# Kernel tuning notes

Hardware: AMD Instinct MI355X
Metric: run time of the kernel (lower is better)

## Reference

```python
import jax, jax.numpy as jnp
import numpy as np

NPG = 39      # nodes per graph, from (1+8+64+9)*(39+1)=3280 = lin1 in_features
NEG_SLOPE = 0.2


def gat_conv(x, src, dst, W, a_src, a_dst, b, n):
    """PyG GATConv, heads=1, self-loops already appended to (src, dst).
    x:[N,Fin] W:[Fin,Fout] a_src/a_dst:[Fout] b:[Fout] -> [N,Fout]"""
    h = x @ W                                        # [N,Fout]
    e = jax.nn.leaky_relu(h[src] @ a_src + h[dst] @ a_dst, NEG_SLOPE)  # [E]
    m = jax.lax.stop_gradient(jax.ops.segment_max(e, dst, num_segments=n))
    w = jnp.exp(e - m[dst])
    denom = jax.ops.segment_sum(w, dst, num_segments=n)
    alpha = w / (denom[dst] + 1e-16)                 # segment softmax per target node
    out = jax.ops.segment_sum(alpha[:, None] * h[src], dst, num_segments=n)
    return out + b


def setup_inputs() -> dict:
    key = jax.random.key(0)
    ks = jax.random.split(key, 20)
    B, DEG = 4096, 8
    N = B * NPG
    E = N * DEG
    x = jax.random.normal(ks[0], (N, 1), dtype=jnp.float32)
    # block-diagonal edges: each node emits DEG edges to random nodes in SAME graph
    src = jnp.repeat(jnp.arange(N, dtype=jnp.int64), DEG)
    offs = (src // NPG) * NPG
    dst = offs + jax.random.randint(ks[1], (E,), 0, NPG, dtype=jnp.int64)
    edge_index = jnp.stack([src, dst])
    batch_vec = jnp.repeat(jnp.arange(B, dtype=jnp.int64), NPG)

    def glorot(k, shape):
        fan = shape[0] + (shape[1] if len(shape) > 1 else 1)
        s = jnp.sqrt(6.0 / fan)
        return jax.random.uniform(k, shape, jnp.float32, -s, s)

    p = {
        'W1': glorot(ks[2], (1, 8)),   'a1s': glorot(ks[3], (8,)),  'a1d': glorot(ks[4], (8,)),  'b1': jnp.zeros((8,), jnp.float32),
        'W2': glorot(ks[5], (8, 64)),  'a2s': glorot(ks[6], (64,)), 'a2d': glorot(ks[7], (64,)), 'b2': jnp.zeros((64,), jnp.float32),
        'W3': glorot(ks[8], (64, 9)),  'a3s': glorot(ks[9], (9,)),  'a3d': glorot(ks[10], (9,)), 'b3': jnp.zeros((9,), jnp.float32),
        'lW1': glorot(ks[11], (3280, 5000)), 'lb1': jnp.zeros((5000,), jnp.float32),
        'lW2': glorot(ks[12], (5000, 1024)), 'lb2': jnp.zeros((1024,), jnp.float32),
        'lW3': glorot(ks[13], (1024, 9)),    'lb3': jnp.zeros((9,), jnp.float32),
    }
    return {'x': x, 'edge_index': edge_index, 'batch_vec': batch_vec, **p}


def reference(x, edge_index, batch_vec,
              W1, a1s, a1d, b1, W2, a2s, a2d, b2, W3, a3s, a3d, b3,
              lW1, lb1, lW2, lb2, lW3, lb3):
    N = x.shape[0]
    B = N // NPG
    loops = jnp.arange(N, dtype=edge_index.dtype)
    src = jnp.concatenate([edge_index[0], loops])   # GATConv add_self_loops=True
    dst = jnp.concatenate([edge_index[1], loops])

    res = x.reshape(B, -1)                                    # [B,39]
    out0 = jax.ops.segment_max(x, batch_vec, num_segments=B)  # [B,1]

    h1 = jax.nn.relu(gat_conv(x, src, dst, W1, a1s, a1d, b1, N))   # dropout = eval no-op
    res1 = h1.reshape(B, -1)                                   # [B,312]
    out1 = jax.ops.segment_max(h1, batch_vec, num_segments=B)

    h2 = jax.nn.relu(gat_conv(h1, src, dst, W2, a2s, a2d, b2, N))
    res2 = h2.reshape(B, -1)                                   # [B,2496]
    out2 = jax.ops.segment_max(h2, batch_vec, num_segments=B)

    h3 = jax.nn.relu(gat_conv(h2, src, dst, W3, a3s, a3d, b3, N))
    res3 = h3.reshape(B, -1)                                   # [B,351]
    out3 = jax.ops.segment_max(h3, batch_vec, num_segments=B)

    f = jnp.concatenate([res, res1, res2, res3, out0, out1, out2, out3], axis=1)  # [B,3280]
    f = jax.nn.relu(f @ lW1 + lb1)
    f = jax.nn.relu(f @ lW2 + lb2)
    return f @ lW3 + lb3                                       # [B,9]
```

## Files before the change

kernel.cpp:

```cpp
#include <hip/hip_runtime.h>
#include <hip/hip_bf16.h>
#include <hip/hip_fp16.h>
#include <stdint.h>


typedef float f32x4 __attribute__((ext_vector_type(4)));
typedef short bf16x8 __attribute__((ext_vector_type(8)));
typedef _Float16 f16x8 __attribute__((ext_vector_type(8)));

__device__ __forceinline__ unsigned fenc(float f) {
  int s = __float_as_int(f);
  return s < 0 ? ~(unsigned)s : ((unsigned)s | 0x80000000u);
}
__device__ __forceinline__ float fdec(unsigned u) {
  return (u & 0x80000000u) ? __int_as_float((int)(u & 0x7fffffffu))
                           : __int_as_float(~(int)u);
}


__global__ __launch_bounds__(128) void gnn_block(
    const float* __restrict__ x,
    const int* __restrict__ esrc, const int* __restrict__ edst,
    const float* __restrict__ W1, const float* __restrict__ a1s, const float* __restrict__ a1d, const float* __restrict__ b1,
    const float* __restrict__ W2, const float* __restrict__ a2s, const float* __restrict__ a2d, const float* __restrict__ b2,
    const float* __restrict__ W3, const float* __restrict__ a3s, const float* __restrict__ a3d, const float* __restrict__ b3,
    __hip_bfloat16* __restrict__ fA)
{
  __shared__ __align__(16) float A[1720];
  __shared__ __align__(16) __half Hh2[2816];
  __shared__ __align__(16) __half h1h[320];
  __shared__ __align__(16) float HfT[400];
  __shared__ __align__(16) float sW3T[616];
  __shared__ __align__(16) float xbuf[40];
  __shared__ __align__(16) float a2buf[128];
  __shared__ float sarr[40], darr[40], den[40];
  __shared__ unsigned umax[40];
  __shared__ unsigned umx[132];
  __shared__ float a3sb[12], a3db[12], b3b[12];

  const int tid = threadIdx.x, g = blockIdx.x, w = tid >> 6, f = tid & 63;

  const int rt = g >> 7, mi = (g >> 4) & 7, lrow = g & 15;
  const size_t gbase = (size_t)rt * 52 * 8192 + (size_t)(mi * 2) * 512 + (size_t)lrow * 8;
#define COLADDR(c) (gbase + (size_t)((c) >> 6) * 8192 + (size_t)(((c) >> 5) & 1) * 512 \
                    + (size_t)(((c) >> 3) & 3) * 128 + ((c) & 7))

  for (int i = tid; i < 576; i += 128) { int k = i / 9, f3 = i - 9 * k; sW3T[f3 * 68 + k] = W3[i]; }
  a2buf[tid] = (tid < 64) ? a2s[tid] : a2d[tid - 64];
  if (tid < 9) { a3sb[tid] = a3s[tid]; a3db[tid] = a3d[tid]; b3b[tid] = b3[tid]; }
  for (int i = tid; i < 132; i += 128) umx[i] = 0u;
  for (int i = tid; i < 430; i += 128) *(f32x4*)&A[i * 4] = (f32x4){0.f, 0.f, 0.f, 0.f};
  for (int i = tid; i < 400; i += 128) HfT[i] = 0.f;
  if (tid < 40) { den[tid] = 0.f; umax[tid] = 0u; xbuf[tid] = 0.f; }

  float xv = 0.f;
  if (tid < 39) { xv = x[g * 39 + tid]; xbuf[tid] = xv; fA[COLADDR(tid)] = __float2bfloat16(xv); }

  int els[3], eld[3];
  const int eb = g * 312, nb0 = g * 39;
#pragma unroll
  for (int it = 0; it < 3; ++it) {
    int e = it * 128 + tid, ls = -1, ld = 0;
    if (e < 351) {
      if (e < 312) { ls = esrc[eb + e] - nb0; ld = edst[eb + e] - nb0; }
      else         { ls = e - 312; ld = ls; }
    }
    els[it] = ls; eld[it] = ld;
  }
  float c_s = 0.f, c_d = 0.f;
  const float w1r = W1[tid & 7], b1r = b1[tid & 7];
#pragma unroll
  for (int ff = 0; ff < 8; ++ff) { float wv = W1[ff]; c_s += wv * a1s[ff]; c_d += wv * a1d[ff]; }
  __syncthreads();

  if (tid < 39) atomicMax(&umx[0], fenc(xv));
  float ee[3];
#pragma unroll
  for (int it = 0; it < 3; ++it) {
    if (els[it] >= 0) {
      float e = xbuf[els[it]] * c_s + xbuf[eld[it]] * c_d;
      e = (e > 0.f) ? e : 0.2f * e;
      ee[it] = e;
      atomicMax(&umax[eld[it]], fenc(e));
    }
  }
  __syncthreads();
#pragma unroll
  for (int it = 0; it < 3; ++it) {
    if (els[it] >= 0) {
      float wv = __expf(ee[it] - fdec(umax[eld[it]]));
      atomicAdd(&den[eld[it]], wv);
      atomicAdd(&A[eld[it] * 44 + els[it]], wv);
    }
  }
  __syncthreads();
  if (tid < 39) {
    const float* Ar = &A[tid * 44];
    float q = 0.f;
#pragma unroll
    for (int c = 0; c < 10; ++c) {
      f32x4 a4 = *(const f32x4*)&Ar[c * 4];
      f32x4 x4 = *(const f32x4*)&xbuf[c * 4];
      q += a4.x * x4.x + a4.y * x4.y + a4.z * x4.z + a4.w * x4.w;
    }
    sarr[tid] = q * (1.f / (den[tid] + 1e-16f));
  }
  __syncthreads();
#pragma unroll
  for (int it = 0; it < 3; ++it) {
    int slot = it * 128 + tid;
    if (slot < 312) {
      int i = slot >> 3, fi = slot & 7;
      float v = fmaxf(sarr[i] * w1r + b1r, 0.f);
      h1h[slot] = __float2half(v);
      fA[COLADDR(39 + slot)] = __float2bfloat16(v);
      atomicMax(&umx[1 + fi], fenc(v));
    }
  }
  __syncthreads();

  float ht2r[40];
  {
    float w2k[8];
#pragma unroll
    for (int k = 0; k < 8; ++k) w2k[k] = W2[k * 64 + f];
#pragma unroll
    for (int i = 0; i < 39; ++i) {
      f16x8 hr = *(const f16x8*)&h1h[i * 8];
      float hv = 0.f;
#pragma unroll
      for (int k = 0; k < 8; ++k) hv += (float)hr[k] * w2k[k];
      ht2r[i] = hv;
    }
    ht2r[39] = 0.f;
#pragma unroll
    for (int i = 0; i < 39; ++i) {
      if ((i < 20) ? (w == 0) : (w == 1))
        Hh2[i * 72 + f] = __float2half(ht2r[i]);
    }
    for (int i = tid; i < 430; i += 128) *(f32x4*)&A[i * 4] = (f32x4){0.f, 0.f, 0.f, 0.f};
    if (tid < 39) { den[tid] = 0.f; umax[tid] = 0u; }
  }
  __syncthreads();
  {
    int node = f;
    if (node < 39) {
      const float* ab = a2buf + (tid & 64);
      const __half* hr = &Hh2[node * 72];
      float s = 0.f;
#pragma unroll
      for (int c = 0; c < 8; ++c) {
        f16x8 hv = *(const f16x8*)&hr[c * 8];
        f32x4 a0 = *(const f32x4*)&ab[c * 8];
        f32x4 a1 = *(const f32x4*)&ab[c * 8 + 4];
        s += (float)hv[0] * a0.x + (float)hv[1] * a0.y + (float)hv[2] * a0.z + (float)hv[3] * a0.w
           + (float)hv[4] * a1.x + (float)hv[5] * a1.y + (float)hv[6] * a1.z + (float)hv[7] * a1.w;
      }
      if (tid < 64) sarr[node] = s; else darr[node] = s;
    }
  }
  __syncthreads();
#pragma unroll
  for (int it = 0; it < 3; ++it) {
    if (els[it] >= 0) {
      float e = sarr[els[it]] + darr[eld[it]];
      e = (e > 0.f) ? e : 0.2f * e;
      ee[it] = e;
      atomicMax(&umax[eld[it]], fenc(e));
    }
  }
  __syncthreads();
#pragma unroll
  for (int it = 0; it < 3; ++it) {
    if (els[it] >= 0) {
      float wv = __expf(ee[it] - fdec(umax[eld[it]]));
      atomicAdd(&den[eld[it]], wv);
      atomicAdd(&A[eld[it] * 44 + els[it]], wv);
    }
  }
  __syncthreads();
  {
    const float b2r = b2[f];
    for (int it = 0; it < 20; ++it) {
      int i = it * 2 + w;
      if (i < 39) {
        float inv = 1.f / (den[i] + 1e-16f);
        const float* Ar = &A[i * 44];
        float acc = 0.f;
#pragma unroll
        for (int c = 0; c < 10; ++c) {
          f32x4 a4 = *(const f32x4*)&Ar[c * 4];
          acc += a4.x * ht2r[c * 4] + a4.y * ht2r[c * 4 + 1]
               + a4.z * ht2r[c * 4 + 2] + a4.w * ht2r[c * 4 + 3];
        }
        float v = fmaxf(acc * inv + b2r, 0.f);
        Hh2[i * 72 + f] = __float2half(v);
        fA[COLADDR(351 + i * 64 + f)] = __float2bfloat16(v);
        atomicMax(&umx[9 + f], fenc(v));
      }
    }
  }
  __syncthreads();

  {
#pragma unroll
    for (int it = 0; it < 3; ++it) {
      int slot = it * 128 + tid;
      if (slot < 351) {
        int i = slot / 9, f3 = slot - 9 * i;
        const __half* hr = &Hh2[i * 72];
        const float* wr = &sW3T[f3 * 68];
        float acc = 0.f;
#pragma unroll
        for (int c = 0; c < 8; ++c) {
          f16x8 hv = *(const f16x8*)&hr[c * 8];
          f32x4 w0 = *(const f32x4*)&wr[c * 8];
          f32x4 w1 = *(const f32x4*)&wr[c * 8 + 4];
          acc += (float)hv[0] * w0.x + (float)hv[1] * w0.y + (float)hv[2] * w0.z + (float)hv[3] * w0.w
               + (float)hv[4] * w1.x + (float)hv[5] * w1.y + (float)hv[6] * w1.z + (float)hv[7] * w1.w;
        }
        HfT[f3 * 44 + i] = acc;
      }
    }
    for (int i = tid; i < 430; i += 128) *(f32x4*)&A[i * 4] = (f32x4){0.f, 0.f, 0.f, 0.f};
    if (tid < 39) { den[tid] = 0.f; umax[tid] = 0u; }
  }
  __syncthreads();
  {
    int node = f;
    if (node < 39) {
      const float* av = (tid < 64) ? a3sb : a3db;
      float s = 0.f;
#pragma unroll
      for (int f3 = 0; f3 < 9; ++f3) s += HfT[f3 * 44 + node] * av[f3];
      if (tid < 64) sarr[node] = s; else darr[node] = s;
    }
  }
  __syncthreads();
#pragma unroll
  for (int it = 0; it < 3; ++it) {
    if (els[it] >= 0) {
      float e = sarr[els[it]] + darr[eld[it]];
      e = (e > 0.f) ? e : 0.2f * e;
      ee[it] = e;
      atomicMax(&umax[eld[it]], fenc(e));
    }
  }
  __syncthreads();
#pragma unroll
  for (int it = 0; it < 3; ++it) {
    if (els[it] >= 0) {
      float wv = __expf(ee[it] - fdec(umax[eld[it]]));
      atomicAdd(&den[eld[it]], wv);
      atomicAdd(&A[eld[it] * 44 + els[it]], wv);
    }
  }
  __syncthreads();
#pragma unroll
  for (int it = 0; it < 3; ++it) {
    int slot = it * 128 + tid;
    if (slot < 351) {
      int i = slot / 9, f3 = slot - 9 * i;
      float inv = 1.f / (den[i] + 1e-16f);
      const float* Ar = &A[i * 44];
      const float* Hr = &HfT[f3 * 44];
      float acc = 0.f;
#pragma unroll
      for (int c = 0; c < 10; ++c) {
        f32x4 a4 = *(const f32x4*)&Ar[c * 4];
        f32x4 h4 = *(const f32x4*)&Hr[c * 4];
        acc += a4.x * h4.x + a4.y * h4.y + a4.z * h4.z + a4.w * h4.w;
      }
      float v = fmaxf(acc * inv + b3b[f3], 0.f);
      fA[COLADDR(2847 + slot)] = __float2bfloat16(v);
      atomicMax(&umx[73 + f3], fenc(v));
    }
  }
  __syncthreads();

  if (tid < 130) {
    int c = 3198 + tid;
    float v = (tid < 82) ? fdec(umx[tid]) : 0.f;
    fA[COLADDR(c)] = __float2bfloat16(v);
  }
#undef COLADDR
}


__global__ __launch_bounds__(256) void conv_tiled(
    const float* __restrict__ W, short* __restrict__ WT,
    int K0, int N0, int KT)
{
  __shared__ float t[64][68];
  const int kb = blockIdx.x * 64, nb = blockIdx.y * 64;
  const int tid = threadIdx.x;
  const int tx = tid & 15, ty = tid >> 4;
#pragma unroll
  for (int r = 0; r < 4; ++r) {
    int k = kb + ty + r * 16, n = nb + tx * 4;
    float4 v = make_float4(0.f, 0.f, 0.f, 0.f);
    if (k < K0 && n < N0) v = *(const float4*)&W[(size_t)k * N0 + n];
    t[ty + r * 16][tx * 4 + 0] = v.x; t[ty + r * 16][tx * 4 + 1] = v.y;
    t[ty + r * 16][tx * 4 + 2] = v.z; t[ty + r * 16][tx * 4 + 3] = v.w;
  }
  __syncthreads();
  const int nl = tid >> 2, kc0 = tid & 3;
#pragma unroll
  for (int h = 0; h < 2; ++h) {
    int kc = kc0 + h * 4;
    int n = nb + nl, k = kb + kc * 8;
    union { bf16x8 v; __hip_bfloat16 b[8]; } z;
#pragma unroll
    for (int j = 0; j < 8; ++j) z.b[j] = __float2bfloat16(t[kc * 8 + j][nl]);
    int rt = n >> 7, mi = (n >> 4) & 7, lr = n & 15;
    int kt = k >> 6, kq = (k >> 5) & 1, lc = (k >> 3) & 3;
    size_t addr = ((((size_t)rt * KT) + kt) * 16 + mi * 2 + kq) * 512 + ((size_t)lr + 16 * lc) * 8;
    *(bf16x8*)&WT[addr] = z.v;
  }
}


__device__ __forceinline__ void gld_lds16(const void* gptr, void* l) {
  typedef const __attribute__((address_space(1))) unsigned int GU;
  typedef __attribute__((address_space(3))) unsigned int LU;
  __builtin_amdgcn_global_load_lds((GU*)gptr, (LU*)l, 16, 0, 0);
}

template<int MODE>
__global__ __launch_bounds__(256) void gemm_tiled(
    const short* __restrict__ A, const short* __restrict__ B,
    const float* __restrict__ bias, int Nreal,
    void* __restrict__ Cout, int Nn, int KT, int ktPerSplit, int outKT)
{
  __shared__ __align__(16) short lA[8192];
  __shared__ __align__(16) short lB[8192];
  const int tid = threadIdx.x;
  const int w = tid >> 6, L = tid & 63;
  const int lrow = L & 15, lch = L >> 4;
  const int mt = blockIdx.y, nt = blockIdx.x;
  const int mw = (w >> 1) * 4, nw = (w & 1) * 4;
  const int kt0 = blockIdx.z * ktPerSplit, kt1 = kt0 + ktPerSplit;

  const short* Ab = A + ((size_t)mt * KT) * 8192 + (size_t)L * 8;
  const short* Bb = B + ((size_t)nt * KT) * 8192 + (size_t)L * 8;

  f32x4 acc[4][4] = {};

  for (int kt = kt0; kt < kt1; ++kt) {
    const short* Ak = Ab + (size_t)kt * 8192;
    const short* Bk = Bb + (size_t)kt * 8192;
#pragma unroll
    for (int j = 0; j < 4; ++j) {
      int st = w * 4 + j;
      gld_lds16(Ak + st * 512, &lA[st * 512]);
      gld_lds16(Bk + st * 512, &lB[st * 512]);
    }
    __syncthreads();
#pragma unroll
    for (int kk = 0; kk < 2; ++kk) {
      bf16x8 af[4], bfr[4];
#pragma unroll
      for (int i = 0; i < 4; ++i) {
        af[i]  = *(const bf16x8*)&lA[((mw + i) * 2 + kk) * 512 + L * 8];
        bfr[i] = *(const bf16x8*)&lB[((nw + i) * 2 + kk) * 512 + L * 8];
      }
#pragma unroll
      for (int i = 0; i < 4; ++i)
#pragma unroll
        for (int j = 0; j < 4; ++j)
          acc[i][j] = __builtin_amdgcn_mfma_f32_16x16x32_bf16(af[i], bfr[j], acc[i][j], 0, 0, 0);
    }
    __syncthreads();
  }

  if (MODE == 0) {
    __hip_bfloat16* C = (__hip_bfloat16*)Cout;
#pragma unroll
    for (int j = 0; j < 4; ++j) {
      int n = nt * 128 + (nw + j) * 16 + lrow;
      float bn = (n < Nreal) ? bias[n] : 0.f;
      int kt = n >> 6, kq = (n >> 5) & 1, lc2 = (n >> 3) & 3, j2 = n & 7;
#pragma unroll
      for (int i = 0; i < 4; ++i) {
        int mi = mw + i;
        size_t base = ((((size_t)mt * outKT + kt) * 16) + mi * 2 + kq) * 512
                      + (size_t)(lch * 4) * 8 + (size_t)lc2 * 128 + j2;
#pragma unroll
        for (int r = 0; r < 4; ++r)
          C[base + r * 8] = __float2bfloat16(fmaxf(acc[i][j][r] + bn, 0.f));
      }
    }
  } else {
    float* P = (float*)Cout + (size_t)blockIdx.z * 4096 * 1024;
#pragma unroll
    for (int j = 0; j < 4; ++j) {
      int n = nt * 128 + (nw + j) * 16 + lrow;
#pragma unroll
      for (int i = 0; i < 4; ++i)
#pragma unroll
        for (int r = 0; r < 4; ++r) {
          int m = mt * 128 + (mw + i) * 16 + lch * 4 + r;
          P[(size_t)m * Nn + n] = acc[i][j][r];
        }
    }
  }
}


__global__ __launch_bounds__(256) void gemm3_fused(
    const float* __restrict__ P,
    const float* __restrict__ b2v,
    const float* __restrict__ W3,
    const float* __restrict__ b3v,
    float* __restrict__ out)
{
  __shared__ float sW3[9 * 1024];
  int tid = threadIdx.x;
  for (int i = tid; i < 9216; i += 256) { int k = i / 9, j = i - 9 * k; sW3[j * 1024 + k] = W3[i]; }
  __syncthreads();
  int row = blockIdx.x * 4 + (tid >> 6);
  int lane = tid & 63;
  const float* p0 = P + (size_t)row * 1024;
  const float* p1 = p0 + (size_t)4096 * 1024;
  float acc[9] = {0, 0, 0, 0, 0, 0, 0, 0, 0};
  for (int t = 0; t < 16; ++t) {
    int k = lane + 64 * t;
    float c = fmaxf(p0[k] + p1[k] + b2v[k], 0.f);
#pragma unroll
    for (int j = 0; j < 9; ++j) acc[j] += c * sW3[j * 1024 + k];
  }
#pragma unroll
  for (int j = 0; j < 9; ++j) {
    float v = acc[j];
    v += __shfl_down(v, 32, 64);
    v += __shfl_down(v, 16, 64);
    v += __shfl_down(v, 8, 64);
    v += __shfl_down(v, 4, 64);
    v += __shfl_down(v, 2, 64);
    v += __shfl_down(v, 1, 64);
    if (lane == 0) out[(size_t)row * 9 + j] = v + b3v[j];
  }
}


extern "C" void kernel_launch(void* const* d_in, const int* in_sizes, int n_in,
                              void* d_out, int out_size, void* d_ws, size_t ws_size,
                              hipStream_t stream)
{
  const float* x   = (const float*)d_in[0];
  const int*   ei  = (const int*)d_in[1];
  const float* W1  = (const float*)d_in[3];
  const float* a1s = (const float*)d_in[4];
  const float* a1d = (const float*)d_in[5];
  const float* b1  = (const float*)d_in[6];
  const float* W2  = (const float*)d_in[7];
  const float* a2s = (const float*)d_in[8];
  const float* a2d = (const float*)d_in[9];
  const float* b2  = (const float*)d_in[10];
  const float* W3  = (const float*)d_in[11];
  const float* a3s = (const float*)d_in[12];
  const float* a3d = (const float*)d_in[13];
  const float* b3  = (const float*)d_in[14];
  const float* lW1 = (const float*)d_in[15];
  const float* lb1 = (const float*)d_in[16];
  const float* lW2 = (const float*)d_in[17];
  const float* lb2 = (const float*)d_in[18];
  const float* lW3 = (const float*)d_in[19];
  const float* lb3 = (const float*)d_in[20];

  const int E = 4096 * 39 * 8;
  const int* esrc = ei;
  const int* edst = ei + E;

  short* fA  = (short*)d_ws;
  short* W1T = fA  + (size_t)4096 * 3328;
  short* C1  = W1T + (size_t)5120 * 3328;
  short* W2T = C1  + (size_t)4096 * 5120;
  float* P   = (float*)d_ws;

  conv_tiled<<<dim3(3328 / 64, 5120 / 64), 256, 0, stream>>>(lW1, W1T, 3280, 5000, 52);
  conv_tiled<<<dim3(5120 / 64, 1024 / 64), 256, 0, stream>>>(lW2, W2T, 5000, 1024, 80);
  gnn_block<<<4096, 128, 0, stream>>>(x, esrc, edst,
                                      W1, a1s, a1d, b1, W2, a2s, a2d, b2, W3, a3s, a3d, b3,
                                      (__hip_bfloat16*)fA);
  gemm_tiled<0><<<dim3(40, 32, 1), 256, 0, stream>>>(fA, W1T, lb1, 5000, C1, 5120, 52, 52, 80);
  gemm_tiled<1><<<dim3(8, 32, 2), 256, 0, stream>>>(C1, W2T, nullptr, 1024, P, 1024, 80, 40, 0);
  gemm3_fused<<<1024, 256, 0, stream>>>(P, lb2, lW3, lb3, (float*)d_out);
}
```

Measured before the change: 492.3 us.

## Fuse weight conversion kernels and GNN block into one interleaved prep kernel

New measurement: 538.7 us. 1.09x slower.

```diff
diff --git a/kernel.cpp b/kernel.cpp
--- a/kernel.cpp
+++ b/kernel.cpp
@@ -18,27 +18,96 @@
 }
 
 
-__global__ __launch_bounds__(128) void gnn_block(
+struct __align__(16) GnnSmem {
+  float A[1720];
+  __half Hh2[2816];
+  __half h1h[320];
+  float HfT[400];
+  float sW3T[616];
+  float xbuf[40];
+  float a2buf[128];
+  float sarr[40], darr[40], den[40];
+  unsigned umax[40];
+  unsigned umx[132];
+  float a3sb[12], a3db[12], b3b[12];
+};
+struct __align__(16) ConvSmem { float t[64][68]; };
+union __align__(16) PrepSmem { GnnSmem g; ConvSmem c; };
+
+__device__ __forceinline__ void conv_tile(
+    const float* __restrict__ W, short* __restrict__ WT,
+    int ktile, int ntile, int K0, int N0, int KT,
+    float (*t)[68], int tid)
+{
+  const int kb = ktile * 64, nb = ntile * 64;
+  const int tx = tid & 15, ty = tid >> 4;
+#pragma unroll
+  for (int r = 0; r < 8; ++r) {
+    int k = kb + ty + r * 8, n = nb + tx * 4;
+    float4 v = make_float4(0.f, 0.f, 0.f, 0.f);
+    if (k < K0 && n < N0) v = *(const float4*)&W[(size_t)k * N0 + n];
+    t[ty + r * 8][tx * 4 + 0] = v.x; t[ty + r * 8][tx * 4 + 1] = v.y;
+    t[ty + r * 8][tx * 4 + 2] = v.z; t[ty + r * 8][tx * 4 + 3] = v.w;
+  }
+  __syncthreads();
+  const int nl = tid >> 1, kc0 = tid & 1;
+#pragma unroll
+  for (int h = 0; h < 4; ++h) {
+    int kc = kc0 + h * 2;
+    int n = nb + nl, k = kb + kc * 8;
+    union { bf16x8 v; __hip_bfloat16 b[8]; } z;
+#pragma unroll
+    for (int j = 0; j < 8; ++j) z.b[j] = __float2bfloat16(t[kc * 8 + j][nl]);
+    int rt = n >> 7, mi = (n >> 4) & 7, lr = n & 15;
+    int kt = k >> 6, kq = (k >> 5) & 1, lc = (k >> 3) & 3;
+    size_t addr = ((((size_t)rt * KT) + kt) * 16 + mi * 2 + kq) * 512 + ((size_t)lr + 16 * lc) * 8;
+    *(bf16x8*)&WT[addr] = z.v;
+  }
+}
+
+__global__ __launch_bounds__(128) void prep_fused(
     const float* __restrict__ x,
     const int* __restrict__ esrc, const int* __restrict__ edst,
     const float* __restrict__ W1, const float* __restrict__ a1s, const float* __restrict__ a1d, const float* __restrict__ b1,
     const float* __restrict__ W2, const float* __restrict__ a2s, const float* __restrict__ a2d, const float* __restrict__ b2,
     const float* __restrict__ W3, const float* __restrict__ a3s, const float* __restrict__ a3d, const float* __restrict__ b3,
-    __hip_bfloat16* __restrict__ fA)
+    const float* __restrict__ lW1, const float* __restrict__ lW2,
+    __hip_bfloat16* __restrict__ fA, short* __restrict__ W1T, short* __restrict__ W2T)
 {
-  __shared__ __align__(16) float A[1720];
-  __shared__ __align__(16) __half Hh2[2816];
-  __shared__ __align__(16) __half h1h[320];
-  __shared__ __align__(16) float HfT[400];
-  __shared__ __align__(16) float sW3T[616];
-  __shared__ __align__(16) float xbuf[40];
-  __shared__ __align__(16) float a2buf[128];
-  __shared__ float sarr[40], darr[40], den[40];
-  __shared__ unsigned umax[40];
-  __shared__ unsigned umx[132];
-  __shared__ float a3sb[12], a3db[12], b3b[12];
-
-  const int tid = threadIdx.x, g = blockIdx.x, w = tid >> 6, f = tid & 63;
+  __shared__ PrepSmem sm;
+  const int tid = threadIdx.x;
+  const int bid = blockIdx.x;
+
+  int g = -1, ci = -1;
+  if ((bid & 1) == 0) {
+    int h = bid >> 1;
+    if (h < 4096) g = h; else ci = 4768 + (h - 4096);
+  } else {
+    ci = bid >> 1;
+  }
+
+  if (g < 0) {
+    if (ci < 4160) {
+      conv_tile(lW1, W1T, ci % 52, ci / 52, 3280, 5000, 52, sm.c.t, tid);
+    } else {
+      int c2 = ci - 4160;
+      conv_tile(lW2, W2T, c2 % 80, c2 / 80, 5000, 1024, 80, sm.c.t, tid);
+    }
+    return;
+  }
+
+  float* A = sm.g.A;
+  __half* Hh2 = sm.g.Hh2;
+  __half* h1h = sm.g.h1h;
+  float* HfT = sm.g.HfT;
+  float* sW3T = sm.g.sW3T;
+  float* xbuf = sm.g.xbuf;
+  float* a2buf = sm.g.a2buf;
+  float* sarr = sm.g.sarr; float* darr = sm.g.darr; float* den = sm.g.den;
+  unsigned* umax = sm.g.umax; unsigned* umx = sm.g.umx;
+  float* a3sb = sm.g.a3sb; float* a3db = sm.g.a3db; float* b3b = sm.g.b3b;
+
+  const int w = tid >> 6, f = tid & 63;
 
   const int rt = g >> 7, mi = (g >> 4) & 7, lrow = g & 15;
   const size_t gbase = (size_t)rt * 52 * 8192 + (size_t)(mi * 2) * 512 + (size_t)lrow * 8;
@@ -284,39 +353,6 @@
     fA[COLADDR(c)] = __float2bfloat16(v);
   }
 #undef COLADDR
-}
-
-
-__global__ __launch_bounds__(256) void conv_tiled(
-    const float* __restrict__ W, short* __restrict__ WT,
-    int K0, int N0, int KT)
-{
-  __shared__ float t[64][68];
-  const int kb = blockIdx.x * 64, nb = blockIdx.y * 64;
-  const int tid = threadIdx.x;
-  const int tx = tid & 15, ty = tid >> 4;
-#pragma unroll
-  for (int r = 0; r < 4; ++r) {
-    int k = kb + ty + r * 16, n = nb + tx * 4;
-    float4 v = make_float4(0.f, 0.f, 0.f, 0.f);
-    if (k < K0 && n < N0) v = *(const float4*)&W[(size_t)k * N0 + n];
-    t[ty + r * 16][tx * 4 + 0] = v.x; t[ty + r * 16][tx * 4 + 1] = v.y;
-    t[ty + r * 16][tx * 4 + 2] = v.z; t[ty + r * 16][tx * 4 + 3] = v.w;
-  }
-  __syncthreads();
-  const int nl = tid >> 2, kc0 = tid & 3;
-#pragma unroll
-  for (int h = 0; h < 2; ++h) {
-    int kc = kc0 + h * 4;
-    int n = nb + nl, k = kb + kc * 8;
-    union { bf16x8 v; __hip_bfloat16 b[8]; } z;
-#pragma unroll
-    for (int j = 0; j < 8; ++j) z.b[j] = __float2bfloat16(t[kc * 8 + j][nl]);
-    int rt = n >> 7, mi = (n >> 4) & 7, lr = n & 15;
-    int kt = k >> 6, kq = (k >> 5) & 1, lc = (k >> 3) & 3;
-    size_t addr = ((((size_t)rt * KT) + kt) * 16 + mi * 2 + kq) * 512 + ((size_t)lr + 16 * lc) * 8;
-    *(bf16x8*)&WT[addr] = z.v;
-  }
 }
 
 
@@ -478,11 +514,9 @@
   short* W2T = C1  + (size_t)4096 * 5120;
   float* P   = (float*)d_ws;
 
-  conv_tiled<<<dim3(3328 / 64, 5120 / 64), 256, 0, stream>>>(lW1, W1T, 3280, 5000, 52);
-  conv_tiled<<<dim3(5120 / 64, 1024 / 64), 256, 0, stream>>>(lW2, W2T, 5000, 1024, 80);
-  gnn_block<<<4096, 128, 0, stream>>>(x, esrc, edst,
-                                      W1, a1s, a1d, b1, W2, a2s, a2d, b2, W3, a3s, a3d, b3,
-                                      (__hip_bfloat16*)fA);
+  prep_fused<<<9536, 128, 0, stream>>>(x, esrc, edst,
+                                       W1, a1s, a1d, b1, W2, a2s, a2d, b2, W3, a3s, a3d, b3,
+                                       lW1, lW2, (__hip_bfloat16*)fA, W1T, W2T);
   gemm_tiled<0><<<dim3(40, 32, 1), 256, 0, stream>>>(fA, W1T, lb1, 5000, C1, 5120, 52, 52, 80);
   gemm_tiled<1><<<dim3(8, 32, 2), 256, 0, stream>>>(C1, W2T, nullptr, 1024, P, 1024, 80, 40, 0);
   gemm3_fused<<<1024, 256, 0, stream>>>(P, lb2, lW3, lb3, (float*)d_out);
```

## Merge weight conversions into one launch, split-K 4 ways with fp16 partials

Applied to the files above, without the earlier changes.

After: 482.1 us. 2.1% less time.

```diff
diff --git a/kernel.cpp b/kernel.cpp
--- a/kernel.cpp
+++ b/kernel.cpp
@@ -287,13 +287,17 @@
 }
 
 
-__global__ __launch_bounds__(256) void conv_tiled(
-    const float* __restrict__ W, short* __restrict__ WT,
-    int K0, int N0, int KT)
+__global__ __launch_bounds__(256) void conv_all(
+    const float* __restrict__ lW1, const float* __restrict__ lW2,
+    short* __restrict__ W1T, short* __restrict__ W2T)
 {
   __shared__ float t[64][68];
-  const int kb = blockIdx.x * 64, nb = blockIdx.y * 64;
-  const int tid = threadIdx.x;
+  const int bid = blockIdx.x, tid = threadIdx.x;
+  const float* W; short* WT; int ktile, ntile, K0, N0, KT;
+  if (bid < 4160) { W = lW1; WT = W1T; ktile = bid % 52; ntile = bid / 52; K0 = 3280; N0 = 5000; KT = 52; }
+  else { int c2 = bid - 4160; W = lW2; WT = W2T; ktile = c2 % 80; ntile = c2 / 80; K0 = 5000; N0 = 1024; KT = 80; }
+
+  const int kb = ktile * 64, nb = ntile * 64;
   const int tx = tid & 15, ty = tid >> 4;
 #pragma unroll
   for (int r = 0; r < 4; ++r) {
@@ -391,7 +395,7 @@
       }
     }
   } else {
-    float* P = (float*)Cout + (size_t)blockIdx.z * 4096 * 1024;
+    __half* P = (__half*)Cout + (size_t)blockIdx.z * 4096 * 1024;
 #pragma unroll
     for (int j = 0; j < 4; ++j) {
       int n = nt * 128 + (nw + j) * 16 + lrow;
@@ -400,7 +404,7 @@
 #pragma unroll
         for (int r = 0; r < 4; ++r) {
           int m = mt * 128 + (mw + i) * 16 + lch * 4 + r;
-          P[(size_t)m * Nn + n] = acc[i][j][r];
+          P[(size_t)m * Nn + n] = __float2half(acc[i][j][r]);
         }
     }
   }
@@ -408,7 +412,7 @@
 
 
 __global__ __launch_bounds__(256) void gemm3_fused(
-    const float* __restrict__ P,
+    const __half* __restrict__ P,
     const float* __restrict__ b2v,
     const float* __restrict__ W3,
     const float* __restrict__ b3v,
@@ -420,12 +424,14 @@
   __syncthreads();
   int row = blockIdx.x * 4 + (tid >> 6);
   int lane = tid & 63;
-  const float* p0 = P + (size_t)row * 1024;
-  const float* p1 = p0 + (size_t)4096 * 1024;
+  const __half* p0 = P + (size_t)row * 1024;
+  const size_t S = (size_t)4096 * 1024;
   float acc[9] = {0, 0, 0, 0, 0, 0, 0, 0, 0};
   for (int t = 0; t < 16; ++t) {
     int k = lane + 64 * t;
-    float c = fmaxf(p0[k] + p1[k] + b2v[k], 0.f);
+    float c = __half2float(p0[k]) + __half2float(p0[k + S])
+            + __half2float(p0[k + 2 * S]) + __half2float(p0[k + 3 * S]) + b2v[k];
+    c = fmaxf(c, 0.f);
 #pragma unroll
     for (int j = 0; j < 9; ++j) acc[j] += c * sW3[j * 1024 + k];
   }
@@ -476,14 +482,13 @@
   short* W1T = fA  + (size_t)4096 * 3328;
   short* C1  = W1T + (size_t)5120 * 3328;
   short* W2T = C1  + (size_t)4096 * 5120;
-  float* P   = (float*)d_ws;
-
-  conv_tiled<<<dim3(3328 / 64, 5120 / 64), 256, 0, stream>>>(lW1, W1T, 3280, 5000, 52);
-  conv_tiled<<<dim3(5120 / 64, 1024 / 64), 256, 0, stream>>>(lW2, W2T, 5000, 1024, 80);
+  __half* P  = (__half*)d_ws;
+
+  conv_all<<<5440, 256, 0, stream>>>(lW1, lW2, W1T, W2T);
   gnn_block<<<4096, 128, 0, stream>>>(x, esrc, edst,
                                       W1, a1s, a1d, b1, W2, a2s, a2d, b2, W3, a3s, a3d, b3,
                                       (__hip_bfloat16*)fA);
   gemm_tiled<0><<<dim3(40, 32, 1), 256, 0, stream>>>(fA, W1T, lb1, 5000, C1, 5120, 52, 52, 80);
-  gemm_tiled<1><<<dim3(8, 32, 2), 256, 0, stream>>>(C1, W2T, nullptr, 1024, P, 1024, 80, 40, 0);
+  gemm_tiled<1><<<dim3(8, 32, 4), 256, 0, stream>>>(C1, W2T, nullptr, 1024, P, 1024, 80, 20, 0);
   gemm3_fused<<<1024, 256, 0, stream>>>(P, lb2, lW3, lb3, (float*)d_out);
 }
```
